# Kernel optimization log

Hardware: AMD Instinct MI355X
Metric: run time of the kernel (lower is better)

## Reference

```python
import jax, jax.numpy as jnp
import numpy as np
from jax import lax

T, X, H = 16384, 512, 1024
A_SCALE, A_IDENTITY = 0.1, 0.9


def setup_inputs() -> dict:
    key = jax.random.key(0)
    k1, k2, k3 = jax.random.split(key, 3)
    x_seq = jax.random.normal(k1, (T, X), dtype=jnp.float32)
    h0 = jnp.zeros((H,), dtype=jnp.float32)
    # A_raw is orthogonal-initialized in the module; a random normal matrix
    # is fine as a correctness baseline (orthogonalize for numerical parity).
    A_raw = jax.random.normal(k2, (H, H), dtype=jnp.float32)
    A_raw, _ = jnp.linalg.qr(A_raw)
    B = jax.random.normal(k3, (H, X), dtype=jnp.float32) * (1.0 / np.sqrt(X))  # lecun_normal
    c = jnp.zeros((H,), dtype=jnp.float32)
    return {"x_seq": x_seq, "h0": h0, "A_raw": A_raw, "B": B, "c": c}


def reference(x_seq, h0, A_raw, B, c):
    # A = a_identity * I + a_scale * A_raw
    A = A_IDENTITY * jnp.eye(H, dtype=A_raw.dtype) + A_SCALE * A_raw
    # Precompute input projections for all timesteps in one GEMM: [T, H]
    Bx = x_seq @ B.T + c

    def step(h, bx_t):
        h_new = jnp.tanh(A @ h + bx_t)
        return h_new, h_new

    _, h_all = lax.scan(step, h0, Bx)
    return h_all
```

## Files before the change

### kernel.cpp

```cpp
#include <hip/hip_runtime.h>
#include <math.h>


#define T_STEPS 16384
#define XD 512
#define HD 1024

typedef unsigned int uint32x4 __attribute__((ext_vector_type(4)));

#define DPP_ADD(v, ctrl, rm)                                          \
    v += __int_as_float(__builtin_amdgcn_update_dpp(                  \
        0, __float_as_int(v), ctrl, rm, 0xf, true))

__device__ __forceinline__ float fast_tanh(float x)
{
    const float e = __expf(2.0f * x);
    return 1.0f - 2.0f / (e + 1.0f);
}

__global__ __launch_bounds__(256) void gemm_bx_kernel(
    const float* __restrict__ x, const float* __restrict__ B,
    const float* __restrict__ c, float* __restrict__ out)
{
    __shared__ __align__(16) float xs[32][68];
    __shared__ __align__(16) float bs[32][68];

    const int tid = threadIdx.x;
    const int t0 = blockIdx.x * 64;
    const int i0 = blockIdx.y * 64;
    const int tx = tid & 15;
    const int ty = tid >> 4;
    const int lr = tid >> 3;
    const int lc = (tid & 7) << 2;

    float acc[4][4] = {{0.f}};

    for (int k0 = 0; k0 < XD; k0 += 32) {
        const float4 xa = *(const float4*)&x[(size_t)(t0 + lr) * XD + k0 + lc];
        const float4 xb = *(const float4*)&x[(size_t)(t0 + lr + 32) * XD + k0 + lc];
        const float4 ba = *(const float4*)&B[(size_t)(i0 + lr) * XD + k0 + lc];
        const float4 bb = *(const float4*)&B[(size_t)(i0 + lr + 32) * XD + k0 + lc];
        __syncthreads();
        xs[lc + 0][lr] = xa.x; xs[lc + 1][lr] = xa.y; xs[lc + 2][lr] = xa.z; xs[lc + 3][lr] = xa.w;
        xs[lc + 0][lr + 32] = xb.x; xs[lc + 1][lr + 32] = xb.y; xs[lc + 2][lr + 32] = xb.z; xs[lc + 3][lr + 32] = xb.w;
        bs[lc + 0][lr] = ba.x; bs[lc + 1][lr] = ba.y; bs[lc + 2][lr] = ba.z; bs[lc + 3][lr] = ba.w;
        bs[lc + 0][lr + 32] = bb.x; bs[lc + 1][lr + 32] = bb.y; bs[lc + 2][lr + 32] = bb.z; bs[lc + 3][lr + 32] = bb.w;
        __syncthreads();
        #pragma unroll
        for (int k = 0; k < 32; ++k) {
            const float4 av = *(const float4*)&xs[k][ty << 2];
            const float4 bv = *(const float4*)&bs[k][tx << 2];
            const float am[4] = {av.x, av.y, av.z, av.w};
            const float bn[4] = {bv.x, bv.y, bv.z, bv.w};
            #pragma unroll
            for (int m = 0; m < 4; ++m)
                #pragma unroll
                for (int n = 0; n < 4; ++n)
                    acc[m][n] = fmaf(am[m], bn[n], acc[m][n]);
        }
    }

    #pragma unroll
    for (int m = 0; m < 4; ++m) {
        const int trow = t0 + (ty << 2) + m;
        #pragma unroll
        for (int n = 0; n < 4; ++n) {
            const int icol = i0 + (tx << 2) + n;
            out[(size_t)trow * HD + icol] = acc[m][n] + c[icol];
        }
    }
}

__global__ void init_slots_kernel(unsigned long long* slots, const float* h0)
{
    const int i = threadIdx.x;
    union { float f; unsigned u; } v; v.f = h0[i];
    slots[3 * HD + i] = (unsigned long long)v.u;
    slots[0 * HD + i] = 0xFFFFFFFF00000000ull;
    slots[1 * HD + i] = 0xFFFFFFFF00000000ull;
    slots[2 * HD + i] = 0xFFFFFFFF00000000ull;
}

__global__ __launch_bounds__(512) void rnn_scan_kernel(
    const float* __restrict__ A_raw, float* out,
    unsigned long long* slots)
{
    const int tid = threadIdx.x;
    const int bid = blockIdx.x;
    const int wave = tid >> 6;
    const int lane = tid & 63;
    const int r0 = (bid << 4) + (wave << 1);

    __shared__ float hlds[2][HD];

    float aw0[16], aw1[16];
    #pragma unroll
    for (int j = 0; j < 16; ++j) {
        const int k = lane + (j << 6);
        float v0 = 0.1f * A_raw[(size_t)r0 * HD + k];
        float v1 = 0.1f * A_raw[(size_t)(r0 + 1) * HD + k];
        if (k == r0) v0 += 0.9f;
        if (k == r0 + 1) v1 += 0.9f;
        aw0[j] = v0; aw1[j] = v1;
    }

    float2 bxn = *(const float2*)&out[r0];

    for (int t = 0; t < T_STEPS; ++t) {
        const float2 bx = bxn;

        const unsigned long long* sp =
            slots + ((size_t)((t + 3) & 3) << 10) + (tid << 1);
        uint32x4 s;
        do {
            asm volatile(
                "global_load_dwordx4 %0, %1, off sc0 sc1\n\t"
                "s_waitcnt vmcnt(0)"
                : "=v"(s) : "v"(sp));
        } while (s.y != (unsigned)t || s.w != (unsigned)t);

        union { unsigned u; float f; } c0, c1; c0.u = s.x; c1.u = s.z;
        *(float2*)&hlds[t & 1][tid << 1] = make_float2(c0.f, c1.f);
        __syncthreads();

        const int tn = (t + 1 < T_STEPS) ? (t + 1) : t;
        bxn = *(const float2*)&out[(size_t)tn * HD + r0];

        const float* hl = hlds[t & 1];
        float p0 = 0.f, p1 = 0.f;
        #pragma unroll
        for (int j = 0; j < 16; ++j) {
            const float hvj = hl[lane + (j << 6)];
            p0 = fmaf(aw0[j], hvj, p0);
            p1 = fmaf(aw1[j], hvj, p1);
        }

        DPP_ADD(p0, 0x111, 0xf); DPP_ADD(p1, 0x111, 0xf);
        DPP_ADD(p0, 0x112, 0xf); DPP_ADD(p1, 0x112, 0xf);
        DPP_ADD(p0, 0x114, 0xf); DPP_ADD(p1, 0x114, 0xf);
        DPP_ADD(p0, 0x118, 0xf); DPP_ADD(p1, 0x118, 0xf);
        DPP_ADD(p0, 0x142, 0xa); DPP_ADD(p1, 0x142, 0xa);
        DPP_ADD(p0, 0x143, 0xc); DPP_ADD(p1, 0x143, 0xc);

        if (lane == 63) {
            const float h0n = fast_tanh(p0 + bx.x);
            const float h1n = fast_tanh(p1 + bx.y);
            union { float f; unsigned u; } u0, u1; u0.f = h0n; u1.f = h1n;
            uint32x4 pkt;
            pkt.x = u0.u; pkt.y = (unsigned)(t + 1);
            pkt.z = u1.u; pkt.w = (unsigned)(t + 1);
            unsigned long long* dp = slots + ((size_t)(t & 3) << 10) + r0;
            asm volatile(
                "global_store_dwordx4 %0, %1, off sc0 sc1"
                :: "v"(dp), "v"(pkt) : "memory");
            *(float2*)&out[(size_t)t * HD + r0] = make_float2(h0n, h1n);
        }
    }
}

extern "C" void kernel_launch(void* const* d_in, const int* in_sizes, int n_in,
                              void* d_out, int out_size, void* d_ws, size_t ws_size,
                              hipStream_t stream)
{
    const float* x     = (const float*)d_in[0];
    const float* h0    = (const float*)d_in[1];
    const float* A_raw = (const float*)d_in[2];
    const float* B     = (const float*)d_in[3];
    const float* c     = (const float*)d_in[4];
    float* out = (float*)d_out;
    unsigned long long* slots = (unsigned long long*)d_ws;

    dim3 gemm_grid(T_STEPS / 64, HD / 64);
    gemm_bx_kernel<<<gemm_grid, 256, 0, stream>>>(x, B, c, out);
    init_slots_kernel<<<1, HD, 0, stream>>>(slots, h0);
    rnn_scan_kernel<<<64, 512, 0, stream>>>(A_raw, out, slots);
}
```

Measured before the change: 20.73 ms.

## Pipeline cross-block flag polling via async global-to-LDS loads

Replaces the serial spin loop, where each poll issues a coherent global load and waits for it, with a rotating set of four in-flight global_load_lds requests into a per-wave LDS scratch. The wave checks whichever slot has landed and reissues loads while waiting, falling back to the old blocking poll after a bounded number of attempts. The goal is to cut the latency of detecting the previous step's hidden state in the latency-bound sequential scan. It adds complex manual waitcnt handling and relies on global_load_lds ordering and coherence semantics, so stale reads or races are a risk.

```diff
diff --git a/kernel.cpp b/kernel.cpp
--- a/kernel.cpp
+++ b/kernel.cpp
@@ -92,6 +92,7 @@
     const int r0 = (bid << 4) + (wave << 1);
 
     __shared__ float hlds[2][HD];
+    __shared__ __align__(16) unsigned pscr[8][4][256];
 
     float aw0[16], aw1[16];
     #pragma unroll
@@ -104,27 +105,66 @@
         aw0[j] = v0; aw1[j] = v1;
     }
 
+    #pragma unroll
+    for (int s = 0; s < 4; ++s) {
+        pscr[wave][s][(lane << 2) + 1] = 0xFFFFFFFFu;
+        pscr[wave][s][(lane << 2) + 3] = 0xFFFFFFFFu;
+    }
+    __syncthreads();
+
     float2 bxn = *(const float2*)&out[r0];
 
     for (int t = 0; t < T_STEPS; ++t) {
-        const float2 bx = bxn;
-
         const unsigned long long* sp =
             slots + ((size_t)((t + 3) & 3) << 10) + (tid << 1);
-        uint32x4 s;
-        do {
-            asm volatile(
-                "global_load_dwordx4 %0, %1, off sc0 sc1\n\t"
-                "s_waitcnt vmcnt(0)"
-                : "=v"(s) : "v"(sp));
-        } while (s.y != (unsigned)t || s.w != (unsigned)t);
-
-        union { unsigned u; float f; } c0, c1; c0.u = s.x; c1.u = s.z;
-        *(float2*)&hlds[t & 1][tid << 1] = make_float2(c0.f, c1.f);
-        __syncthreads();
+
+        asm volatile("s_waitcnt vmcnt(3)" ::: "memory");
+        __builtin_amdgcn_sched_barrier(0);
+
+        #pragma unroll
+        for (int s2 = 0; s2 < 4; ++s2)
+            __builtin_amdgcn_global_load_lds(sp, &pscr[wave][s2][0], 16, 0, 17);
+
+        float2 hv;
+        for (int i = 0; ; ++i) {
+            const int slot = i & 3;
+            asm volatile("s_waitcnt vmcnt(3)" ::: "memory");
+            __builtin_amdgcn_sched_barrier(0);
+            uint32x4 pk;
+            const unsigned la =
+                (unsigned)(size_t)&pscr[wave][slot][lane << 2];
+            asm volatile("ds_read_b128 %0, %1\n\t"
+                         "s_waitcnt lgkmcnt(0)"
+                         : "=&v"(pk) : "v"(la));
+            __builtin_amdgcn_sched_barrier(0);
+            if (pk.y == (unsigned)t && pk.w == (unsigned)t) {
+                hv = make_float2(__uint_as_float(pk.x), __uint_as_float(pk.z));
+                break;
+            }
+            if (i == 12) {
+                asm volatile("s_waitcnt vmcnt(0)" ::: "memory");
+                uint32x4 s3;
+                do {
+                    asm volatile(
+                        "global_load_dwordx4 %0, %1, off sc0 sc1\n\t"
+                        "s_waitcnt vmcnt(0)"
+                        : "=v"(s3) : "v"(sp));
+                } while (s3.y != (unsigned)t || s3.w != (unsigned)t);
+                hv = make_float2(__uint_as_float(s3.x), __uint_as_float(s3.z));
+                break;
+            }
+            __builtin_amdgcn_global_load_lds(sp, &pscr[wave][slot][0], 16, 0, 17);
+        }
+
+        const float2 bx = bxn;
+
+        *(float2*)&hlds[t & 1][tid << 1] = make_float2(hv.x, hv.y);
 
         const int tn = (t + 1 < T_STEPS) ? (t + 1) : t;
         bxn = *(const float2*)&out[(size_t)tn * HD + r0];
+
+        asm volatile("s_waitcnt lgkmcnt(0)\n\t"
+                     "s_barrier" ::: "memory");
 
         const float* hl = hlds[t & 1];
         float p0 = 0.f, p1 = 0.f;
@@ -156,6 +196,8 @@
             *(float2*)&out[(size_t)t * HD + r0] = make_float2(h0n, h1n);
         }
     }
+
+    asm volatile("s_waitcnt vmcnt(0)" ::: "memory");
 }
 
 extern "C" void kernel_launch(void* const* d_in, const int* in_sizes, int n_in,
```

After: 33.27 ms. +60.5%, slower.

## Have each wave poll the full hidden state directly instead of sharing via LDS

Applied to the files above, without the earlier changes.

Each wave now polls all 1024 hidden-state slots itself with eight dwordx4 loads per lane, where before the block split the polling across threads and shared the values through LDS. This removes the LDS staging and the per-step __syncthreads barrier, so each wave proceeds as soon as its own view of the state is ready. The A weights are re-indexed to match the new interleaved k layout, and the dot product uses two accumulators per row. In exchange every wave issues 8x more coherent global loads per poll, which adds L2 traffic and contention on the spin loop.

```diff
diff --git a/kernel.cpp b/kernel.cpp
--- a/kernel.cpp
+++ b/kernel.cpp
@@ -11,6 +11,8 @@
 #define DPP_ADD(v, ctrl, rm)                                          \
     v += __int_as_float(__builtin_amdgcn_update_dpp(                  \
         0, __float_as_int(v), ctrl, rm, 0xf, true))
+
+#define VF(u) __uint_as_float(u)
 
 __device__ __forceinline__ float fast_tanh(float x)
 {
@@ -91,49 +93,73 @@
     const int lane = tid & 63;
     const int r0 = (bid << 4) + (wave << 1);
 
-    __shared__ float hlds[2][HD];
-
     float aw0[16], aw1[16];
     #pragma unroll
-    for (int j = 0; j < 16; ++j) {
-        const int k = lane + (j << 6);
-        float v0 = 0.1f * A_raw[(size_t)r0 * HD + k];
-        float v1 = 0.1f * A_raw[(size_t)(r0 + 1) * HD + k];
-        if (k == r0) v0 += 0.9f;
-        if (k == r0 + 1) v1 += 0.9f;
-        aw0[j] = v0; aw1[j] = v1;
-    }
+    for (int j = 0; j < 8; ++j)
+        #pragma unroll
+        for (int b = 0; b < 2; ++b) {
+            const int k = (lane << 1) + (j << 7) + b;
+            float v0 = 0.1f * A_raw[(size_t)r0 * HD + k];
+            float v1 = 0.1f * A_raw[(size_t)(r0 + 1) * HD + k];
+            if (k == r0) v0 += 0.9f;
+            if (k == r0 + 1) v1 += 0.9f;
+            aw0[(j << 1) + b] = v0; aw1[(j << 1) + b] = v1;
+        }
 
     float2 bxn = *(const float2*)&out[r0];
 
     for (int t = 0; t < T_STEPS; ++t) {
+        const unsigned long long* b0 =
+            slots + ((size_t)((t + 3) & 3) << 10) + (lane << 1);
+        const unsigned long long* b1 = b0 + 512;
+        uint32x4 q0, q1, q2, q3, q4, q5, q6, q7;
+        const unsigned tt = (unsigned)t;
+        for (;;) {
+            asm volatile(
+                "global_load_dwordx4 %0, %8, off sc0 sc1\n\t"
+                "global_load_dwordx4 %1, %8, off offset:1024 sc0 sc1\n\t"
+                "global_load_dwordx4 %2, %8, off offset:2048 sc0 sc1\n\t"
+                "global_load_dwordx4 %3, %8, off offset:3072 sc0 sc1\n\t"
+                "global_load_dwordx4 %4, %9, off sc0 sc1\n\t"
+                "global_load_dwordx4 %5, %9, off offset:1024 sc0 sc1\n\t"
+                "global_load_dwordx4 %6, %9, off offset:2048 sc0 sc1\n\t"
+                "global_load_dwordx4 %7, %9, off offset:3072 sc0 sc1\n\t"
+                "s_waitcnt vmcnt(0)"
+                : "=&v"(q0), "=&v"(q1), "=&v"(q2), "=&v"(q3),
+                  "=&v"(q4), "=&v"(q5), "=&v"(q6), "=&v"(q7)
+                : "v"(b0), "v"(b1)
+                : "memory");
+            const int ok =
+                (q0.y == tt) & (q0.w == tt) & (q1.y == tt) & (q1.w == tt) &
+                (q2.y == tt) & (q2.w == tt) & (q3.y == tt) & (q3.w == tt) &
+                (q4.y == tt) & (q4.w == tt) & (q5.y == tt) & (q5.w == tt) &
+                (q6.y == tt) & (q6.w == tt) & (q7.y == tt) & (q7.w == tt);
+            if (__all(ok)) break;
+        }
+
         const float2 bx = bxn;
-
-        const unsigned long long* sp =
-            slots + ((size_t)((t + 3) & 3) << 10) + (tid << 1);
-        uint32x4 s;
-        do {
-            asm volatile(
-                "global_load_dwordx4 %0, %1, off sc0 sc1\n\t"
-                "s_waitcnt vmcnt(0)"
-                : "=v"(s) : "v"(sp));
-        } while (s.y != (unsigned)t || s.w != (unsigned)t);
-
-        union { unsigned u; float f; } c0, c1; c0.u = s.x; c1.u = s.z;
-        *(float2*)&hlds[t & 1][tid << 1] = make_float2(c0.f, c1.f);
-        __syncthreads();
-
         const int tn = (t + 1 < T_STEPS) ? (t + 1) : t;
         bxn = *(const float2*)&out[(size_t)tn * HD + r0];
 
-        const float* hl = hlds[t & 1];
-        float p0 = 0.f, p1 = 0.f;
-        #pragma unroll
-        for (int j = 0; j < 16; ++j) {
-            const float hvj = hl[lane + (j << 6)];
-            p0 = fmaf(aw0[j], hvj, p0);
-            p1 = fmaf(aw1[j], hvj, p1);
-        }
+        float p0a = 0.f, p0b = 0.f, p1a = 0.f, p1b = 0.f;
+        p0a = fmaf(aw0[0],  VF(q0.x), p0a); p0b = fmaf(aw0[1],  VF(q0.z), p0b);
+        p1a = fmaf(aw1[0],  VF(q0.x), p1a); p1b = fmaf(aw1[1],  VF(q0.z), p1b);
+        p0a = fmaf(aw0[2],  VF(q1.x), p0a); p0b = fmaf(aw0[3],  VF(q1.z), p0b);
+        p1a = fmaf(aw1[2],  VF(q1.x), p1a); p1b = fmaf(aw1[3],  VF(q1.z), p1b);
+        p0a = fmaf(aw0[4],  VF(q2.x), p0a); p0b = fmaf(aw0[5],  VF(q2.z), p0b);
+        p1a = fmaf(aw1[4],  VF(q2.x), p1a); p1b = fmaf(aw1[5],  VF(q2.z), p1b);
+        p0a = fmaf(aw0[6],  VF(q3.x), p0a); p0b = fmaf(aw0[7],  VF(q3.z), p0b);
+        p1a = fmaf(aw1[6],  VF(q3.x), p1a); p1b = fmaf(aw1[7],  VF(q3.z), p1b);
+        p0a = fmaf(aw0[8],  VF(q4.x), p0a); p0b = fmaf(aw0[9],  VF(q4.z), p0b);
+        p1a = fmaf(aw1[8],  VF(q4.x), p1a); p1b = fmaf(aw1[9],  VF(q4.z), p1b);
+        p0a = fmaf(aw0[10], VF(q5.x), p0a); p0b = fmaf(aw0[11], VF(q5.z), p0b);
+        p1a = fmaf(aw1[10], VF(q5.x), p1a); p1b = fmaf(aw1[11], VF(q5.z), p1b);
+        p0a = fmaf(aw0[12], VF(q6.x), p0a); p0b = fmaf(aw0[13], VF(q6.z), p0b);
+        p1a = fmaf(aw1[12], VF(q6.x), p1a); p1b = fmaf(aw1[13], VF(q6.z), p1b);
+        p0a = fmaf(aw0[14], VF(q7.x), p0a); p0b = fmaf(aw0[15], VF(q7.z), p0b);
+        p1a = fmaf(aw1[14], VF(q7.x), p1a); p1b = fmaf(aw1[15], VF(q7.z), p1b);
+        float p0 = p0a + p0b;
+        float p1 = p1a + p1b;
 
         DPP_ADD(p0, 0x111, 0xf); DPP_ADD(p1, 0x111, 0xf);
         DPP_ADD(p0, 0x112, 0xf); DPP_ADD(p1, 0x112, 0xf);
```

Result: slower. 42.15 ms (+103.3%).
